# Optimization experiments

Measured on AMD Instinct MI355X. Metric: run time of the kernel, lower is better.

## Reference

```python
import jax, jax.numpy as jnp
import numpy as np
from jax import lax

# ---- constants mirroring Prediction.__init__ kwargs ----
INP = 608
NUM_CLASSES = 20
ALPHA, BETA = 1.0, 0.5
OBJ_T, CONF_T, LOC_T = 0.6, 0.05, 0.5
NMS_T, SIZE_T, SIGMA = 0.1, 0.0, 0.5
TOP_K = 8
M_CAND = 256          # fixed-size candidate cap for jit-compatible NMS
NEG = -1e9            # sentinel for masked scores
ANCHORS = [[(116, 90), (156, 198), (373, 326)],
           [(30, 61), (62, 45), (59, 119)],
           [(10, 13), (16, 30), (33, 23)]]


def _decode(pred, anchors):
    """pred: (B, A, G, G, 6+C) raw level output -> decoded flat tensors."""
    B, A, G, _, C = pred.shape
    stride = INP // G
    xy = jax.nn.sigmoid(pred[..., 0:2])
    g = jnp.arange(G, dtype=pred.dtype)
    gx, gy = jnp.meshgrid(g, g)                      # gx[i,j]=j, gy[i,j]=i (np.meshgrid 'xy')
    off = jnp.stack([gx, gy], axis=-1)[None, None]   # (1,1,G,G,2)
    xy = ALPHA * xy - 0.5 * (ALPHA - 1.0) + off
    anc = jnp.asarray(anchors, dtype=pred.dtype) / stride  # (A,2) scaled to grid units
    wh = jnp.exp(pred[..., 2:4]) * anc[None, :, None, None, :]
    box = jnp.concatenate([xy, wh], axis=-1) * stride       # back to pixel units
    obj = jax.nn.sigmoid(pred[..., 4])
    loc = jax.nn.sigmoid(pred[..., 5])
    clsp = jax.nn.softmax(pred[..., 6:], axis=-1)
    N = A * G * G
    return (box.reshape(B, N, 4), obj.reshape(B, N),
            loc.reshape(B, N), clsp.reshape(B, N, NUM_CLASSES))


def _soft_nms(boxes, s0, cls):
    """Per-image Gaussian soft-NMS (class-aware), +1 pixel IoU convention as in bbox_iou.
    boxes: (M,4) xyxy, s0: (M,) scores (NEG for invalid), cls: (M,) int. Returns kept mask."""
    M = s0.shape[0]

    def step(carry, _):
        s, kept = carry
        j = jnp.argmax(s)
        do = s[j] >= NMS_T
        kept = kept | ((jnp.arange(M) == j) & do)
        bj = boxes[j]
        ix1 = jnp.maximum(bj[0], boxes[:, 0]); iy1 = jnp.maximum(bj[1], boxes[:, 1])
        ix2 = jnp.minimum(bj[2], boxes[:, 2]); iy2 = jnp.minimum(bj[3], boxes[:, 3])
        inter = jnp.maximum(ix2 - ix1 + 1.0, 0.0) * jnp.maximum(iy2 - iy1 + 1.0, 0.0)
        a1 = (bj[2] - bj[0] + 1.0) * (bj[3] - bj[1] + 1.0)
        a2 = (boxes[:, 2] - boxes[:, 0] + 1.0) * (boxes[:, 3] - boxes[:, 1] + 1.0)
        iou = inter / (a1 + a2 - inter + 1e-16)
        decay = jnp.exp(-(iou * iou) / SIGMA)
        s_new = jnp.where(cls == cls[j], s * decay, s).at[j].set(NEG)
        s = jnp.where(do, s_new, s)
        return (s, kept), None

    (_, kept), _ = lax.scan(step, (s0, jnp.zeros(M, dtype=bool)), None, length=M)
    return kept


def _forward(pred_l0, pred_l1, pred_l2):
    parts = [_decode(p, a) for p, a in zip([pred_l0, pred_l1, pred_l2], ANCHORS)]
    box = jnp.concatenate([p[0] for p in parts], axis=1)   # (B,N,4) xywh
    obj = jnp.concatenate([p[1] for p in parts], axis=1)
    loc = jnp.concatenate([p[2] for p in parts], axis=1)
    clsp = jnp.concatenate([p[3] for p in parts], axis=1)

    cx, cy, w, h = box[..., 0], box[..., 1], box[..., 2], box[..., 3]
    x1 = jnp.clip(cx - w / 2, 0.0, INP); y1 = jnp.clip(cy - h / 2, 0.0, INP)
    x2 = jnp.clip(cx + w / 2, 0.0, INP); y2 = jnp.clip(cy + h / 2, 0.0, INP)
    boxes = jnp.stack([x1, y1, x2, y2], axis=-1)            # (B,N,4) xyxy, clamped

    cls_conf = jnp.max(clsp, axis=-1)
    cls_id = jnp.argmax(clsp, axis=-1)
    area = (x2 - x1) * (y2 - y1)
    valid = ((obj >= OBJ_T) & (area >= INP * INP * SIZE_T)
             & (obj * cls_conf >= CONF_T) & (loc >= LOC_T))
    score = (obj * cls_conf) ** BETA * loc ** (1.0 - BETA)
    masked = jnp.where(valid, score, NEG)

    # fixed-size candidate set per image (descending-score sort + cap)
    vals, idx = lax.top_k(masked, M_CAND)                   # (B,M)
    cboxes = jnp.take_along_axis(boxes, idx[..., None], axis=1)
    ccls = jnp.take_along_axis(cls_id, idx, axis=1)
    s0 = jnp.where(vals > NEG / 2, vals, NEG)

    kept = jax.vmap(_soft_nms)(cboxes, s0, ccls)            # (B,M) bool

    # keep_top_k: top_k among kept, ranked by ORIGINAL (pre-decay) score
    fscore = jnp.where(kept, vals, NEG)
    fvals, fidx = lax.top_k(fscore, TOP_K)                  # (B,TOP_K)
    fboxes = jnp.take_along_axis(cboxes, fidx[..., None], axis=1)
    fcls = jnp.take_along_axis(ccls, fidx, axis=1)
    row = jnp.concatenate([fboxes, fvals[..., None],
                           fcls[..., None].astype(fboxes.dtype)], axis=-1)  # (B,K,6)
    ok = fvals > NEG / 2
    return jnp.where(ok[..., None], row, 0.0)


def setup_inputs() -> dict:
    key = jax.random.key(0)
    k0, k1, k2 = jax.random.split(key, 3)
    return {
        "pred_l0": jax.random.normal(k0, (64, 3, 19, 19, 26), dtype=jnp.float32),
        "pred_l1": jax.random.normal(k1, (64, 3, 38, 38, 26), dtype=jnp.float32),
        "pred_l2": jax.random.normal(k2, (64, 3, 76, 76, 26), dtype=jnp.float32),
    }


def reference(pred_l0, pred_l1, pred_l2):
    return _forward(pred_l0, pred_l1, pred_l2)
```

## Files before the change

kernel.cpp:

```cpp
#include <hip/hip_runtime.h>
#include <climits>

constexpr int kB  = 64;
constexpr int kG0 = 19, kG1 = 38, kG2 = 76;
constexpr int kN0 = 3 * kG0 * kG0;
constexpr int kN1 = 3 * kG1 * kG1;
constexpr int kN2 = 3 * kG2 * kG2;
constexpr int kN  = kN0 + kN1 + kN2;
constexpr int kNP = kN + 1;
constexpr int kM  = 256;
constexpr int kTopK = 8;
constexpr float kNEG = -1e9f;

constexpr int kT0 = 5, kT1 = 17, kT2 = 68;
constexpr int kTilesPerImg = kT0 + kT1 + kT2;
constexpr int kGridScore = 1920;
constexpr int kTilesPerBlk = 3;

__constant__ float c_anchors[3][3][2] = {
    {{116.f, 90.f}, {156.f, 198.f}, {373.f, 326.f}},
    {{30.f, 61.f},  {62.f, 45.f},   {59.f, 119.f}},
    {{10.f, 13.f},  {16.f, 30.f},   {33.f, 23.f}},
};

__device__ __forceinline__ float fexpf(float x) { return __expf(x); }
__device__ __forceinline__ float frcpf(float x) { return __builtin_amdgcn_rcpf(x); }
__device__ __forceinline__ float fsigm(float x) { return frcpf(1.0f + __expf(-x)); }

__device__ __forceinline__ float2 nt_load_f2(const float2* p) {
  unsigned long long v = __builtin_nontemporal_load((const unsigned long long*)p);
  union { unsigned long long u; float2 f; } c; c.u = v; return c.f;
}

__device__ __forceinline__ unsigned score_to_key(float s) {
  unsigned fb = __float_as_uint(s);
  unsigned m = (fb & 0x80000000u) ? 0xFFFFFFFFu : 0x80000000u;
  return fb ^ m;
}
__device__ __forceinline__ float key_to_score(unsigned k) {
  unsigned fb = (k & 0x80000000u) ? (k ^ 0x80000000u) : ~k;
  return __uint_as_float(fb);
}

__device__ __forceinline__ const float* cell_ptr(
    const float* p0, const float* p1, const float* p2, int b, int n,
    int& lvl, int& a, int& gi, int& gj, float& stride) {
  const float* src; int G, m;
  if (n < kN0)            { src = p0; G = kG0; lvl = 0; m = n;             stride = 32.f; }
  else if (n < kN0 + kN1) { src = p1; G = kG1; lvl = 1; m = n - kN0;       stride = 16.f; }
  else                    { src = p2; G = kG2; lvl = 2; m = n - kN0 - kN1; stride = 8.f; }
  int gg = G * G;
  a = m / gg;
  int r = m - a * gg;
  gi = r / G;
  gj = r - gi * G;
  return src + (size_t)((((b * 3 + a) * G + gi) * G + gj)) * 26;
}

__device__ __forceinline__ void waveArgmax(float& v, int& i) {
  #pragma unroll
  for (int off = 1; off < 64; off <<= 1) {
    float ov = __shfl_xor(v, off);
    int oi = __shfl_xor(i, off);
    if (ov > v || (ov == v && oi < i)) { v = ov; i = oi; }
  }
}
__device__ __forceinline__ float waveMax(float v) {
  #pragma unroll
  for (int off = 1; off < 64; off <<= 1) v = fmaxf(v, __shfl_xor(v, off));
  return v;
}
__device__ __forceinline__ float sel4f(const float a[4], int q) {
  float r = a[0];
  r = (q == 1) ? a[1] : r;
  r = (q == 2) ? a[2] : r;
  r = (q == 3) ? a[3] : r;
  return r;
}
__device__ __forceinline__ int sel4i(const int a[4], int q) {
  int r = a[0];
  r = (q == 1) ? a[1] : r;
  r = (q == 2) ? a[2] : r;
  r = (q == 3) ? a[3] : r;
  return r;
}

__global__ __launch_bounds__(256) void score_kernel(
    const float* __restrict__ p0, const float* __restrict__ p1, const float* __restrict__ p2,
    unsigned* __restrict__ keys)
{
  __shared__ float2 lds2[2][256 * 13];

  int t = threadIdx.x;

  const float2* g2[kTilesPerBlk]; int nc[kTilesPerBlk], n0[kTilesPerBlk], bb[kTilesPerBlk];
  #pragma unroll
  for (int j = 0; j < kTilesPerBlk; ++j) {
    int tileId = (int)blockIdx.x + j * kGridScore;
    int b = tileId / kTilesPerImg;
    int r = tileId - b * kTilesPerImg;
    const float* slab; int NL, lvlOff, tile;
    if (r < kT0)            { slab = p0; NL = kN0; lvlOff = 0;         tile = r; }
    else if (r < kT0 + kT1) { slab = p1; NL = kN1; lvlOff = kN0;       tile = r - kT0; }
    else                    { slab = p2; NL = kN2; lvlOff = kN0 + kN1; tile = r - kT0 - kT1; }
    int cellBase = tile * 256;
    nc[j] = min(256, NL - cellBase);
    g2[j] = (const float2*)(slab + ((size_t)b * NL + cellBase) * 26);
    n0[j] = lvlOff + cellBase;
    bb[j] = b;
  }

  float2 nxt[13];

  {
    int tot = nc[0] * 13;
    #pragma unroll
    for (int k = 0; k < 13; ++k) {
      int i = t + k * 256;
      if (i < tot) nxt[k] = nt_load_f2(g2[0] + i);
    }
    #pragma unroll
    for (int k = 0; k < 13; ++k) {
      int i = t + k * 256;
      if (i < tot) lds2[0][i] = nxt[k];
    }
  }

  #pragma unroll
  for (int j = 0; j < kTilesPerBlk; ++j) {
    __syncthreads();

    int totN = 0;
    if (j + 1 < kTilesPerBlk) {
      totN = nc[j + 1] * 13;
      #pragma unroll
      for (int k = 0; k < 13; ++k) {
        int i = t + k * 256;
        if (i < totN) nxt[k] = nt_load_f2(g2[j + 1] + i);
      }
    }

    int curNc = nc[j], curN0 = n0[j], curB = bb[j];
    const float2* bufp = &lds2[j & 1][0];
    if (t < curNc) {
      const float2* c2 = &bufp[t * 13];
      float2 ol = c2[2];
      float obj = fsigm(ol.x);
      float loc = fsigm(ol.y);
      float tch[20];
      #pragma unroll
      for (int q = 0; q < 10; ++q) { float2 v = c2[3 + q]; tch[2*q] = v.x; tch[2*q+1] = v.y; }
      float lm = tch[0];
      #pragma unroll
      for (int c = 1; c < 20; ++c) lm = fmaxf(lm, tch[c]);
      float se = 0.f;
      #pragma unroll
      for (int c = 0; c < 20; ++c) se += fexpf(tch[c] - lm);
      float cls_conf = frcpf(se);
      float conf = obj * cls_conf;
      float masked = (obj >= 0.6f && loc >= 0.5f && conf >= 0.05f)
                     ? sqrtf(conf) * sqrtf(loc) : kNEG;
      keys[(size_t)curB * kNP + curN0 + t] = score_to_key(masked);
    }

    if (j + 1 < kTilesPerBlk) {
      float2* dst = &lds2[(j + 1) & 1][0];
      #pragma unroll
      for (int k = 0; k < 13; ++k) {
        int i = t + k * 256;
        if (i < totN) dst[i] = nxt[k];
      }
    }
  }
}

__device__ __forceinline__ void findThresholdBin(
    const int* hist, int NB, int needed,
    int& outB, int& outCumAbove, int& outTotal,
    int* shWave, int* shOut)
{
  int tid = threadIdx.x, lane = tid & 63, w = tid >> 6;
  if (tid == 0) { shOut[0] = -1; shOut[1] = 0; }
  int ipt = (NB + 511) / 512;
  int base = tid * ipt;
  int csum = 0;
  for (int i = 0; i < ipt; ++i) { int bn = base + i; if (bn < NB) csum += hist[bn]; }
  int v = csum;
  #pragma unroll
  for (int off = 1; off < 64; off <<= 1) {
    int tv = __shfl_down(v, off);
    if (lane + off < 64) v += tv;
  }
  if (lane == 0) shWave[w] = v;
  __syncthreads();
  int above = 0, total = 0;
  #pragma unroll
  for (int q = 0; q < 8; ++q) {
    int wt = shWave[q];
    total += wt;
    if (q > w) above += wt;
  }
  int S = v + above;
  if (S >= needed && S - csum < needed) {
    int running = S - csum;
    for (int i = ipt - 1; i >= 0; --i) {
      int bn = base + i; if (bn >= NB) continue;
      int c = hist[bn];
      if (running + c >= needed) { shOut[0] = bn; shOut[1] = running; break; }
      running += c;
    }
  }
  __syncthreads();
  outB = shOut[0]; outCumAbove = shOut[1]; outTotal = total;
  __syncthreads();
}

constexpr int kNV4 = kN / 4;
constexpr int kTail = kN - kNV4*4;

__global__ __launch_bounds__(512) void select_nms_kernel(
    const unsigned* __restrict__ keys,
    const float* __restrict__ p0, const float* __restrict__ p1, const float* __restrict__ p2,
    float* __restrict__ out)
{
  int b = blockIdx.x, tid = threadIdx.x;
  const unsigned* kk = keys + (size_t)b * kNP;
  const uint4* kk4 = (const uint4*)kk;
  const unsigned keyNEG = score_to_key(kNEG);

  __shared__ int hist[4096];
  __shared__ int eqBuf[1024];
  __shared__ int shWave[8], shOut[2];
  __shared__ unsigned sT;
  __shared__ int sCgt;
  __shared__ int ciL[kM];
  __shared__ unsigned ckL[kM];

  for (int i = tid; i < 4096; i += 512) hist[i] = 0;
  __syncthreads();
  for (int x = tid; x < kNV4; x += 512) {
    uint4 v = kk4[x];
    if (v.x >= 0x80000000u) atomicAdd(&hist[v.x >> 20], 1);
    if (v.y >= 0x80000000u) atomicAdd(&hist[v.y >> 20], 1);
    if (v.z >= 0x80000000u) atomicAdd(&hist[v.z >> 20], 1);
    if (v.w >= 0x80000000u) atomicAdd(&hist[v.w >> 20], 1);
  }
  if (tid < kTail) {
    unsigned k = kk[kNV4 * 4 + tid];
    if (k >= 0x80000000u) atomicAdd(&hist[k >> 20], 1);
  }
  __syncthreads();
  int B, cumAbove1, total1;
  findThresholdBin(hist, 4096, kM, B, cumAbove1, total1, shWave, shOut);

  if (total1 < kM) {
    if (tid == 0) { sT = keyNEG; sCgt = total1; }
    __syncthreads();
  } else {
    int needed2 = kM - cumAbove1;
    for (int i = tid; i < 4096; i += 512) hist[i] = 0;
    __syncthreads();
    for (int x = tid; x < kNV4; x += 512) {
      uint4 v = kk4[x];
      if ((int)(v.x >> 20) == B) atomicAdd(&hist[(v.x >> 8) & 0xFFF], 1);
      if ((int)(v.y >> 20) == B) atomicAdd(&hist[(v.y >> 8) & 0xFFF], 1);
      if ((int)(v.z >> 20) == B) atomicAdd(&hist[(v.z >> 8) & 0xFFF], 1);
      if ((int)(v.w >> 20) == B) atomicAdd(&hist[(v.w >> 8) & 0xFFF], 1);
    }
    if (tid < kTail) {
      unsigned k = kk[kNV4 * 4 + tid];
      if ((int)(k >> 20) == B) atomicAdd(&hist[(k >> 8) & 0xFFF], 1);
    }
    __syncthreads();
    int B2, cumAbove2, total2;
    findThresholdBin(hist, 4096, needed2, B2, cumAbove2, total2, shWave, shOut);
    int prefix24 = (B << 12) | B2;
    int needed3 = needed2 - cumAbove2;

    for (int i = tid; i < 256; i += 512) hist[i] = 0;
    __syncthreads();
    for (int x = tid; x < kNV4; x += 512) {
      uint4 v = kk4[x];
      if ((int)(v.x >> 8) == prefix24) atomicAdd(&hist[v.x & 0xFF], 1);
      if ((int)(v.y >> 8) == prefix24) atomicAdd(&hist[v.y & 0xFF], 1);
      if ((int)(v.z >> 8) == prefix24) atomicAdd(&hist[v.z & 0xFF], 1);
      if ((int)(v.w >> 8) == prefix24) atomicAdd(&hist[v.w & 0xFF], 1);
    }
    if (tid < kTail) {
      unsigned k = kk[kNV4 * 4 + tid];
      if ((int)(k >> 8) == prefix24) atomicAdd(&hist[k & 0xFF], 1);
    }
    __syncthreads();
    int B3, cumAbove3, total3;
    findThresholdBin(hist, 256, needed3, B3, cumAbove3, total3, shWave, shOut);
    if (tid == 0) {
      sT = ((unsigned)prefix24 << 8) | (unsigned)B3;
      sCgt = cumAbove1 + cumAbove2 + cumAbove3;
    }
    __syncthreads();
  }

  unsigned T = sT;
  int cgt = sCgt;

  __shared__ int sCnt, eqCnt;
  if (tid == 0) { sCnt = 0; eqCnt = 0; }
  __syncthreads();
  for (int x = tid; x < kNV4; x += 512) {
    uint4 v = kk4[x];
    int i4 = x * 4;
    unsigned kv[4] = {v.x, v.y, v.z, v.w};
    #pragma unroll
    for (int e = 0; e < 4; ++e) {
      unsigned k = kv[e];
      if (k > T) {
        int p = atomicAdd(&sCnt, 1);
        ciL[p] = i4 + e; ckL[p] = k;
      } else if (k == T && T != keyNEG) {
        int p = atomicAdd(&eqCnt, 1); if (p < 1024) eqBuf[p] = i4 + e;
      }
    }
  }
  if (tid < kTail) {
    int x = kNV4 * 4 + tid;
    unsigned k = kk[x];
    if (k > T) {
      int p = atomicAdd(&sCnt, 1);
      ciL[p] = x; ckL[p] = k;
    } else if (k == T && T != keyNEG) {
      int p = atomicAdd(&eqCnt, 1); if (p < 1024) eqBuf[p] = x;
    }
  }
  __syncthreads();

  int needed = kM - cgt;
  if (T == keyNEG) {
    if (tid >= cgt && tid < kM) { ciL[tid] = -1; ckL[tid] = keyNEG; }
  } else {
    int ce = min(eqCnt, 1024);
    if (ce == needed) {
      if (tid < needed) { ciL[cgt + tid] = eqBuf[tid]; ckL[cgt + tid] = T; }
    } else if (tid == 0) {
      for (int q = 0; q < needed; ++q) {
        int mv = INT_MAX, mp = 0;
        for (int x = 0; x < ce; ++x) if (eqBuf[x] < mv) { mv = eqBuf[x]; mp = x; }
        ciL[cgt + q] = mv; ckL[cgt + q] = T; eqBuf[mp] = INT_MAX;
      }
    }
  }
  __syncthreads();

  if (tid >= 64) return;
  int lane = tid;

  float x1[4], y1[4], x2[4], y2[4], val[4], s[4];
  int cls[4];
  bool kept[4];

  #pragma unroll
  for (int q = 0; q < 4; ++q) {
    int slot = q * 64 + lane;
    int n = ciL[slot];
    float sc = key_to_score(ckL[slot]);
    kept[q] = false;
    x1[q] = y1[q] = x2[q] = y2[q] = 0.f;
    cls[q] = 0; val[q] = sc; s[q] = sc;
    if (n >= 0) {
      int lvl, a, gi, gj; float stride;
      const float* p = cell_ptr(p0, p1, p2, b, n, lvl, a, gi, gj, stride);
      const float2* r2 = (const float2*)p;
      float2 c01 = r2[0], c23 = r2[1];
      float cx = (fsigm(c01.x) + (float)gj) * stride;
      float cy = (fsigm(c01.y) + (float)gi) * stride;
      float w = fexpf(c23.x) * c_anchors[lvl][a][0];
      float h = fexpf(c23.y) * c_anchors[lvl][a][1];
      x1[q] = fminf(fmaxf(cx - 0.5f * w, 0.f), 608.f);
      y1[q] = fminf(fmaxf(cy - 0.5f * h, 0.f), 608.f);
      x2[q] = fminf(fmaxf(cx + 0.5f * w, 0.f), 608.f);
      y2[q] = fminf(fmaxf(cy + 0.5f * h, 0.f), 608.f);
      float lm = -3.4e38f; int mc = 0;
      #pragma unroll
      for (int j = 3; j < 13; ++j) {
        float2 v = r2[j];
        int c0 = 2 * (j - 3);
        if (v.x > lm) { lm = v.x; mc = c0; }
        if (v.y > lm) { lm = v.y; mc = c0 + 1; }
      }
      cls[q] = mc;
    }
  }

  float top8[8];
  #pragma unroll
  for (int i = 0; i < 8; ++i) top8[i] = kNEG;
  int keptCount = 0;

  for (int it = 0; it < kM; ++it) {
    float bv = s[0]; int bq = 0;
    #pragma unroll
    for (int q = 1; q < 4; ++q) if (s[q] > bv) { bv = s[q]; bq = q; }
    int bi = bq * 64 + lane;
    waveArgmax(bv, bi);
    if (bv < 0.1f) break;

    int wlane = bi & 63, wq = bi >> 6;
    float jx1 = __shfl(sel4f(x1, wq), wlane);
    float jy1 = __shfl(sel4f(y1, wq), wlane);
    float jx2 = __shfl(sel4f(x2, wq), wlane);
    float jy2 = __shfl(sel4f(y2, wq), wlane);
    float jval = __shfl(sel4f(val, wq), wlane);
    int   cj  = __shfl(sel4i(cls, wq), wlane);

    float a1 = (jx2 - jx1 + 1.0f) * (jy2 - jy1 + 1.0f);
    #pragma unroll
    for (int q = 0; q < 4; ++q) {
      if (cls[q] == cj) {
        float ix1 = fmaxf(jx1, x1[q]), iy1 = fmaxf(jy1, y1[q]);
        float ix2 = fminf(jx2, x2[q]), iy2 = fminf(jy2, y2[q]);
        float inter = fmaxf(ix2 - ix1 + 1.0f, 0.0f) * fmaxf(iy2 - iy1 + 1.0f, 0.0f);
        float a2 = (x2[q] - x1[q] + 1.0f) * (y2[q] - y1[q] + 1.0f);
        float iou = inter / (a1 + a2 - inter + 1e-16f);
        s[q] *= fexpf(-(iou * iou) * 2.0f);
      }
      if (bi == q * 64 + lane) { kept[q] = true; s[q] = kNEG; }
    }

    float v = jval;
    #pragma unroll
    for (int i = 0; i < 8; ++i) { float m = fmaxf(top8[i], v); v = fminf(top8[i], v); top8[i] = m; }
    ++keptCount;
    if (keptCount >= kTopK) {
      float am = kNEG;
      #pragma unroll
      for (int q = 0; q < 4; ++q) if (s[q] >= 0.1f) am = fmaxf(am, val[q]);
      am = waveMax(am);
      if (am < top8[7]) break;
    }
  }

  float f[4];
  #pragma unroll
  for (int q = 0; q < 4; ++q) f[q] = kept[q] ? val[q] : kNEG;
  for (int k = 0; k < kTopK; ++k) {
    float bv = f[0]; int bq = 0;
    #pragma unroll
    for (int q = 1; q < 4; ++q) if (f[q] > bv) { bv = f[q]; bq = q; }
    int bi = bq * 64 + lane;
    waveArgmax(bv, bi);
    int wlane = bi & 63, wq = bi >> 6;
    if (lane == wlane) {
      float* o = out + (size_t)(b * kTopK + k) * 6;
      if (bv > kNEG * 0.5f) {
        o[0] = sel4f(x1, wq); o[1] = sel4f(y1, wq);
        o[2] = sel4f(x2, wq); o[3] = sel4f(y2, wq);
        o[4] = sel4f(val, wq); o[5] = (float)sel4i(cls, wq);
      } else {
        o[0] = 0.f; o[1] = 0.f; o[2] = 0.f; o[3] = 0.f; o[4] = 0.f; o[5] = 0.f;
      }
    }
    #pragma unroll
    for (int q = 0; q < 4; ++q) if (bi == q * 64 + lane) f[q] = kNEG;
  }
}

extern "C" void kernel_launch(void* const* d_in, const int* in_sizes, int n_in,
                              void* d_out, int out_size, void* d_ws, size_t ws_size,
                              hipStream_t stream) {
  const float* p0 = (const float*)d_in[0];
  const float* p1 = (const float*)d_in[1];
  const float* p2 = (const float*)d_in[2];
  float* out = (float*)d_out;

  unsigned* keys = (unsigned*)d_ws;

  score_kernel<<<kGridScore, 256, 0, stream>>>(p0, p1, p2, keys);
  select_nms_kernel<<<kB, 512, 0, stream>>>(keys, p0, p1, p2, out);
}
```

Before: 230.1 us.

## Build first-pass histogram in score kernel and compact radix-select candidates into LDS pool

The score kernel now builds the per-image top-12-bit key histogram in global memory with atomics, so the select kernel no longer needs its first full pass over the keys. The select kernel then makes a single pass over the keys. It collects keys above the threshold bin directly and stores the threshold-bin keys in an LDS pool, and the remaining radix refinement runs over that pool instead of re-scanning the global keys. The LDS staging also switches to float4 loads when the tile is 16-byte aligned. The costs are a memset, global atomics in the hot score kernel, and more shared memory in the select kernel, which may reduce occupancy.

```diff
diff --git a/kernel.cpp b/kernel.cpp
--- a/kernel.cpp
+++ b/kernel.cpp
@@ -1,5 +1,6 @@
 #include <hip/hip_runtime.h>
 #include <climits>
+#include <cstdint>
 
 constexpr int kB  = 64;
 constexpr int kG0 = 19, kG1 = 38, kG2 = 76;
@@ -11,6 +12,7 @@
 constexpr int kM  = 256;
 constexpr int kTopK = 8;
 constexpr float kNEG = -1e9f;
+constexpr int kHB = 4096;
 
 constexpr int kT0 = 5, kT1 = 17, kT2 = 68;
 constexpr int kTilesPerImg = kT0 + kT1 + kT2;
@@ -23,6 +25,8 @@
     {{10.f, 13.f},  {16.f, 30.f},   {33.f, 23.f}},
 };
 
+typedef float f4_t __attribute__((ext_vector_type(4)));
+
 __device__ __forceinline__ float fexpf(float x) { return __expf(x); }
 __device__ __forceinline__ float frcpf(float x) { return __builtin_amdgcn_rcpf(x); }
 __device__ __forceinline__ float fsigm(float x) { return frcpf(1.0f + __expf(-x)); }
@@ -30,6 +34,9 @@
 __device__ __forceinline__ float2 nt_load_f2(const float2* p) {
   unsigned long long v = __builtin_nontemporal_load((const unsigned long long*)p);
   union { unsigned long long u; float2 f; } c; c.u = v; return c.f;
+}
+__device__ __forceinline__ f4_t nt_load_f4(const f4_t* p) {
+  return __builtin_nontemporal_load(p);
 }
 
 __device__ __forceinline__ unsigned score_to_key(float s) {
@@ -87,13 +94,15 @@
 
 __global__ __launch_bounds__(256) void score_kernel(
     const float* __restrict__ p0, const float* __restrict__ p1, const float* __restrict__ p2,
-    unsigned* __restrict__ keys)
+    unsigned* __restrict__ keys, int* __restrict__ gHist)
 {
-  __shared__ float2 lds2[2][256 * 13];
+  __shared__ float lds[2][256 * 26];
 
   int t = threadIdx.x;
 
-  const float2* g2[kTilesPerBlk]; int nc[kTilesPerBlk], n0[kTilesPerBlk], bb[kTilesPerBlk];
+  const float* gb[kTilesPerBlk];
+  int nc[kTilesPerBlk], nfl[kTilesPerBlk], n0[kTilesPerBlk], bb[kTilesPerBlk];
+  bool al16[kTilesPerBlk];
   #pragma unroll
   for (int j = 0; j < kTilesPerBlk; ++j) {
     int tileId = (int)blockIdx.x + j * kGridScore;
@@ -104,46 +113,85 @@
     else if (r < kT0 + kT1) { slab = p1; NL = kN1; lvlOff = kN0;       tile = r - kT0; }
     else                    { slab = p2; NL = kN2; lvlOff = kN0 + kN1; tile = r - kT0 - kT1; }
     int cellBase = tile * 256;
-    nc[j] = min(256, NL - cellBase);
-    g2[j] = (const float2*)(slab + ((size_t)b * NL + cellBase) * 26);
+    nc[j]  = min(256, NL - cellBase);
+    nfl[j] = nc[j] * 26;
+    gb[j]  = slab + ((size_t)b * NL + cellBase) * 26;
+    al16[j] = ((((uintptr_t)gb[j]) & 15) == 0);
     n0[j] = lvlOff + cellBase;
     bb[j] = b;
   }
 
-  float2 nxt[13];
-
-  {
-    int tot = nc[0] * 13;
-    #pragma unroll
-    for (int k = 0; k < 13; ++k) {
-      int i = t + k * 256;
-      if (i < tot) nxt[k] = nt_load_f2(g2[0] + i);
-    }
-    #pragma unroll
-    for (int k = 0; k < 13; ++k) {
-      int i = t + k * 256;
-      if (i < tot) lds2[0][i] = nxt[k];
-    }
-  }
+  float sreg[28];
+
+  auto stageLoad = [&](int j) {
+    const float* g = gb[j]; int nf = nfl[j];
+    if (al16[j]) {
+      int n4 = nf >> 2;
+      #pragma unroll
+      for (int k = 0; k < 7; ++k) {
+        int i = t + k * 256;
+        if (i < n4) {
+          f4_t v = nt_load_f4((const f4_t*)g + i);
+          sreg[4*k] = v[0]; sreg[4*k+1] = v[1]; sreg[4*k+2] = v[2]; sreg[4*k+3] = v[3];
+        }
+      }
+      if ((nf & 3) && t == 0) {
+        float2 v = nt_load_f2((const float2*)g + (n4 << 1));
+        sreg[26] = v.x; sreg[27] = v.y;
+      }
+    } else {
+      int n2 = nf >> 1;
+      #pragma unroll
+      for (int k = 0; k < 13; ++k) {
+        int i = t + k * 256;
+        if (i < n2) {
+          float2 v = nt_load_f2((const float2*)g + i);
+          sreg[2*k] = v.x; sreg[2*k+1] = v.y;
+        }
+      }
+    }
+  };
+  auto stageWrite = [&](int j, float* dst) {
+    int nf = nfl[j];
+    if (al16[j]) {
+      int n4 = nf >> 2;
+      f4_t* d4 = (f4_t*)dst;
+      #pragma unroll
+      for (int k = 0; k < 7; ++k) {
+        int i = t + k * 256;
+        if (i < n4) {
+          f4_t w; w[0] = sreg[4*k]; w[1] = sreg[4*k+1]; w[2] = sreg[4*k+2]; w[3] = sreg[4*k+3];
+          d4[i] = w;
+        }
+      }
+      if ((nf & 3) && t == 0) {
+        float2* d2 = (float2*)dst;
+        float2 w; w.x = sreg[26]; w.y = sreg[27];
+        d2[n4 << 1] = w;
+      }
+    } else {
+      int n2 = nf >> 1;
+      float2* d2 = (float2*)dst;
+      #pragma unroll
+      for (int k = 0; k < 13; ++k) {
+        int i = t + k * 256;
+        if (i < n2) { float2 w; w.x = sreg[2*k]; w.y = sreg[2*k+1]; d2[i] = w; }
+      }
+    }
+  };
+
+  stageLoad(0);
+  stageWrite(0, &lds[0][0]);
 
   #pragma unroll
   for (int j = 0; j < kTilesPerBlk; ++j) {
     __syncthreads();
 
-    int totN = 0;
-    if (j + 1 < kTilesPerBlk) {
-      totN = nc[j + 1] * 13;
-      #pragma unroll
-      for (int k = 0; k < 13; ++k) {
-        int i = t + k * 256;
-        if (i < totN) nxt[k] = nt_load_f2(g2[j + 1] + i);
-      }
-    }
+    if (j + 1 < kTilesPerBlk) stageLoad(j + 1);
 
     int curNc = nc[j], curN0 = n0[j], curB = bb[j];
-    const float2* bufp = &lds2[j & 1][0];
     if (t < curNc) {
-      const float2* c2 = &bufp[t * 13];
+      const float2* c2 = (const float2*)&lds[j & 1][t * 26];
       float2 ol = c2[2];
       float obj = fsigm(ol.x);
       float loc = fsigm(ol.y);
@@ -160,17 +208,12 @@
       float conf = obj * cls_conf;
       float masked = (obj >= 0.6f && loc >= 0.5f && conf >= 0.05f)
                      ? sqrtf(conf) * sqrtf(loc) : kNEG;
-      keys[(size_t)curB * kNP + curN0 + t] = score_to_key(masked);
-    }
-
-    if (j + 1 < kTilesPerBlk) {
-      float2* dst = &lds2[(j + 1) & 1][0];
-      #pragma unroll
-      for (int k = 0; k < 13; ++k) {
-        int i = t + k * 256;
-        if (i < totN) dst[i] = nxt[k];
-      }
-    }
+      unsigned key = score_to_key(masked);
+      keys[(size_t)curB * kNP + curN0 + t] = key;
+      if (key & 0x80000000u) atomicAdd(&gHist[curB * kHB + (int)(key >> 20)], 1);
+    }
+
+    if (j + 1 < kTilesPerBlk) stageWrite(j + 1, &lds[(j + 1) & 1][0]);
   }
 }
 
@@ -219,7 +262,7 @@
 constexpr int kTail = kN - kNV4*4;
 
 __global__ __launch_bounds__(512) void select_nms_kernel(
-    const unsigned* __restrict__ keys,
+    const unsigned* __restrict__ keys, const int* __restrict__ gHist,
     const float* __restrict__ p0, const float* __restrict__ p1, const float* __restrict__ p2,
     float* __restrict__ out)
 {
@@ -228,127 +271,143 @@
   const uint4* kk4 = (const uint4*)kk;
   const unsigned keyNEG = score_to_key(kNEG);
 
-  __shared__ int hist[4096];
-  __shared__ int eqBuf[1024];
+  constexpr int kPool = 4096;
+  __shared__ int hist[kHB];
   __shared__ int shWave[8], shOut[2];
-  __shared__ unsigned sT;
-  __shared__ int sCgt;
   __shared__ int ciL[kM];
   __shared__ unsigned ckL[kM];
-
-  for (int i = tid; i < 4096; i += 512) hist[i] = 0;
-  __syncthreads();
-  for (int x = tid; x < kNV4; x += 512) {
-    uint4 v = kk4[x];
-    if (v.x >= 0x80000000u) atomicAdd(&hist[v.x >> 20], 1);
-    if (v.y >= 0x80000000u) atomicAdd(&hist[v.y >> 20], 1);
-    if (v.z >= 0x80000000u) atomicAdd(&hist[v.z >> 20], 1);
-    if (v.w >= 0x80000000u) atomicAdd(&hist[v.w >> 20], 1);
-  }
-  if (tid < kTail) {
-    unsigned k = kk[kNV4 * 4 + tid];
-    if (k >= 0x80000000u) atomicAdd(&hist[k >> 20], 1);
-  }
+  __shared__ unsigned pk[kPool];
+  __shared__ int piA[kPool];
+  __shared__ int eqI[256];
+  __shared__ int sCnt, eqCnt, sTie;
+
+  for (int i = tid; i < kHB; i += 512) hist[i] = gHist[(size_t)b * kHB + i];
   __syncthreads();
   int B, cumAbove1, total1;
-  findThresholdBin(hist, 4096, kM, B, cumAbove1, total1, shWave, shOut);
+  findThresholdBin(hist, kHB, kM, B, cumAbove1, total1, shWave, shOut);
+
+  if (tid == 0) { sCnt = 0; eqCnt = 0; sTie = 0; }
+  for (int i = tid; i < kHB; i += 512) hist[i] = 0;
+  __syncthreads();
 
   if (total1 < kM) {
-    if (tid == 0) { sT = keyNEG; sCgt = total1; }
+    for (int x = tid; x < kNV4; x += 512) {
+      uint4 v = kk4[x];
+      int i4 = x * 4;
+      unsigned kv[4] = {v.x, v.y, v.z, v.w};
+      #pragma unroll
+      for (int e = 0; e < 4; ++e) {
+        unsigned k = kv[e];
+        if (k & 0x80000000u) { int p = atomicAdd(&sCnt, 1); ciL[p] = i4 + e; ckL[p] = k; }
+      }
+    }
+    if (tid < kTail) {
+      int x = kNV4 * 4 + tid;
+      unsigned k = kk[x];
+      if (k & 0x80000000u) { int p = atomicAdd(&sCnt, 1); ciL[p] = x; ckL[p] = k; }
+    }
+    __syncthreads();
+    if (tid >= total1 && tid < kM) { ciL[tid] = -1; ckL[tid] = keyNEG; }
     __syncthreads();
   } else {
-    int needed2 = kM - cumAbove1;
-    for (int i = tid; i < 4096; i += 512) hist[i] = 0;
-    __syncthreads();
+    unsigned uB = (unsigned)B;
     for (int x = tid; x < kNV4; x += 512) {
       uint4 v = kk4[x];
-      if ((int)(v.x >> 20) == B) atomicAdd(&hist[(v.x >> 8) & 0xFFF], 1);
-      if ((int)(v.y >> 20) == B) atomicAdd(&hist[(v.y >> 8) & 0xFFF], 1);
-      if ((int)(v.z >> 20) == B) atomicAdd(&hist[(v.z >> 8) & 0xFFF], 1);
-      if ((int)(v.w >> 20) == B) atomicAdd(&hist[(v.w >> 8) & 0xFFF], 1);
+      int i4 = x * 4;
+      unsigned kv[4] = {v.x, v.y, v.z, v.w};
+      #pragma unroll
+      for (int e = 0; e < 4; ++e) {
+        unsigned k = kv[e];
+        unsigned hi = k >> 20;
+        if (hi > uB) { int p = atomicAdd(&sCnt, 1); ciL[p] = i4 + e; ckL[p] = k; }
+        else if (hi == uB) {
+          int p = atomicAdd(&eqCnt, 1);
+          if (p < kPool) { pk[p] = k; piA[p] = i4 + e; }
+          atomicAdd(&hist[(k >> 8) & 0xFFFu], 1);
+        }
+      }
     }
     if (tid < kTail) {
-      unsigned k = kk[kNV4 * 4 + tid];
-      if ((int)(k >> 20) == B) atomicAdd(&hist[(k >> 8) & 0xFFF], 1);
+      int x = kNV4 * 4 + tid;
+      unsigned k = kk[x];
+      unsigned hi = k >> 20;
+      if (hi > uB) { int p = atomicAdd(&sCnt, 1); ciL[p] = x; ckL[p] = k; }
+      else if (hi == uB) {
+        int p = atomicAdd(&eqCnt, 1);
+        if (p < kPool) { pk[p] = k; piA[p] = x; }
+        atomicAdd(&hist[(k >> 8) & 0xFFFu], 1);
+      }
     }
     __syncthreads();
-    int B2, cumAbove2, total2;
-    findThresholdBin(hist, 4096, needed2, B2, cumAbove2, total2, shWave, shOut);
-    int prefix24 = (B << 12) | B2;
-    int needed3 = needed2 - cumAbove2;
-
-    for (int i = tid; i < 256; i += 512) hist[i] = 0;
-    __syncthreads();
-    for (int x = tid; x < kNV4; x += 512) {
-      uint4 v = kk4[x];
-      if ((int)(v.x >> 8) == prefix24) atomicAdd(&hist[v.x & 0xFF], 1);
-      if ((int)(v.y >> 8) == prefix24) atomicAdd(&hist[v.y & 0xFF], 1);
-      if ((int)(v.z >> 8) == prefix24) atomicAdd(&hist[v.z & 0xFF], 1);
-      if ((int)(v.w >> 8) == prefix24) atomicAdd(&hist[v.w & 0xFF], 1);
-    }
-    if (tid < kTail) {
-      unsigned k = kk[kNV4 * 4 + tid];
-      if ((int)(k >> 8) == prefix24) atomicAdd(&hist[k & 0xFF], 1);
-    }
-    __syncthreads();
-    int B3, cumAbove3, total3;
-    findThresholdBin(hist, 256, needed3, B3, cumAbove3, total3, shWave, shOut);
-    if (tid == 0) {
-      sT = ((unsigned)prefix24 << 8) | (unsigned)B3;
-      sCgt = cumAbove1 + cumAbove2 + cumAbove3;
-    }
-    __syncthreads();
-  }
-
-  unsigned T = sT;
-  int cgt = sCgt;
-
-  __shared__ int sCnt, eqCnt;
-  if (tid == 0) { sCnt = 0; eqCnt = 0; }
-  __syncthreads();
-  for (int x = tid; x < kNV4; x += 512) {
-    uint4 v = kk4[x];
-    int i4 = x * 4;
-    unsigned kv[4] = {v.x, v.y, v.z, v.w};
-    #pragma unroll
-    for (int e = 0; e < 4; ++e) {
-      unsigned k = kv[e];
-      if (k > T) {
-        int p = atomicAdd(&sCnt, 1);
-        ciL[p] = i4 + e; ckL[p] = k;
-      } else if (k == T && T != keyNEG) {
-        int p = atomicAdd(&eqCnt, 1); if (p < 1024) eqBuf[p] = i4 + e;
-      }
-    }
-  }
-  if (tid < kTail) {
-    int x = kNV4 * 4 + tid;
-    unsigned k = kk[x];
-    if (k > T) {
-      int p = atomicAdd(&sCnt, 1);
-      ciL[p] = x; ckL[p] = k;
-    } else if (k == T && T != keyNEG) {
-      int p = atomicAdd(&eqCnt, 1); if (p < 1024) eqBuf[p] = x;
-    }
-  }
-  __syncthreads();
-
-  int needed = kM - cgt;
-  if (T == keyNEG) {
-    if (tid >= cgt && tid < kM) { ciL[tid] = -1; ckL[tid] = keyNEG; }
-  } else {
-    int ce = min(eqCnt, 1024);
-    if (ce == needed) {
-      if (tid < needed) { ciL[cgt + tid] = eqBuf[tid]; ckL[cgt + tid] = T; }
-    } else if (tid == 0) {
-      for (int q = 0; q < needed; ++q) {
-        int mv = INT_MAX, mp = 0;
-        for (int x = 0; x < ce; ++x) if (eqBuf[x] < mv) { mv = eqBuf[x]; mp = x; }
-        ciL[cgt + q] = mv; ckL[cgt + q] = T; eqBuf[mp] = INT_MAX;
-      }
-    }
-  }
-  __syncthreads();
+
+    int needed = kM - cumAbove1;
+    int pc = eqCnt;
+
+    if (pc == needed) {
+      if (tid < pc) { ciL[cumAbove1 + tid] = piA[tid]; ckL[cumAbove1 + tid] = pk[tid]; }
+      __syncthreads();
+    } else if (pc <= kPool) {
+      int B2, cA2, tot2;
+      findThresholdBin(hist, kHB, needed, B2, cA2, tot2, shWave, shOut);
+      for (int i = tid; i < 256; i += 512) hist[i] = 0;
+      __syncthreads();
+      for (int i = tid; i < pc; i += 512) {
+        unsigned k = pk[i];
+        int mid = (int)((k >> 8) & 0xFFFu);
+        if (mid > B2) { int p = atomicAdd(&sCnt, 1); ciL[p] = piA[i]; ckL[p] = k; }
+        else if (mid == B2) atomicAdd(&hist[k & 0xFFu], 1);
+      }
+      __syncthreads();
+      int needed3 = needed - cA2;
+      int B3, cA3, tot3;
+      findThresholdBin(hist, 256, needed3, B3, cA3, tot3, shWave, shOut);
+      for (int i = tid; i < pc; i += 512) {
+        unsigned k = pk[i];
+        int mid = (int)((k >> 8) & 0xFFFu);
+        if (mid == B2) {
+          int lo = (int)(k & 0xFFu);
+          if (lo > B3) { int p = atomicAdd(&sCnt, 1); ciL[p] = piA[i]; ckL[p] = k; }
+          else if (lo == B3) { int p = atomicAdd(&sTie, 1); if (p < 256) eqI[p] = piA[i]; }
+        }
+      }
+      __syncthreads();
+      int needed4 = needed3 - cA3;
+      unsigned exactKey = (uB << 20) | ((unsigned)B2 << 8) | (unsigned)B3;
+      int nt_ = sTie;
+      if (nt_ == needed4) {
+        if (tid < needed4) {
+          int base0 = kM - needed4;
+          ciL[base0 + tid] = eqI[tid]; ckL[base0 + tid] = exactKey;
+        }
+      } else if (tid == 0) {
+        int base0 = kM - needed4; int lastI = -1;
+        for (int q = 0; q < needed4; ++q) {
+          int mv = INT_MAX;
+          for (int x = 0; x < pc; ++x) {
+            if (pk[x] == exactKey) { int ix = piA[x]; if (ix > lastI && ix < mv) mv = ix; }
+          }
+          ciL[base0 + q] = mv; ckL[base0 + q] = exactKey; lastI = mv;
+        }
+      }
+      __syncthreads();
+    } else {
+      if (tid == 0) {
+        int base0 = sCnt;
+        unsigned lastK = 0xFFFFFFFFu; int lastI = INT_MAX;
+        for (int q = 0; q < needed; ++q) {
+          unsigned bk = 0u; int bi2 = -1;
+          for (int x = 0; x < kN; ++x) {
+            unsigned k = kk[x];
+            if ((k >> 20) != uB) continue;
+            if (k > lastK || (k == lastK && x <= lastI)) continue;
+            if (bi2 < 0 || k > bk || (k == bk && x < bi2)) { bk = k; bi2 = x; }
+          }
+          ciL[base0 + q] = bi2; ckL[base0 + q] = bk; lastK = bk; lastI = bi2;
+        }
+      }
+      __syncthreads();
+    }
+  }
 
   if (tid >= 64) return;
   int lane = tid;
@@ -472,7 +531,9 @@
   float* out = (float*)d_out;
 
   unsigned* keys = (unsigned*)d_ws;
-
-  score_kernel<<<kGridScore, 256, 0, stream>>>(p0, p1, p2, keys);
-  select_nms_kernel<<<kB, 512, 0, stream>>>(keys, p0, p1, p2, out);
-}
+  int* gHist = (int*)((char*)d_ws + (size_t)kB * kNP * sizeof(unsigned));
+
+  hipMemsetAsync(gHist, 0, (size_t)kB * kHB * sizeof(int), stream);
+  score_kernel<<<kGridScore, 256, 0, stream>>>(p0, p1, p2, keys, gHist);
+  select_nms_kernel<<<kB, 512, 0, stream>>>(keys, gHist, p0, p1, p2, out);
+}
```

After: 261.3 us. 13.5% more time.
